# Optimization experiments

Measured on AMD Instinct MI355X. Metric: run time of the kernel, lower is better.

The kernel has to match this reference:

```python
import jax, jax.numpy as jnp
import numpy as np

N, E, D, O, STEP = 100000, 640000, 128, 64, 10


def setup_inputs() -> dict:
    key = jax.random.key(0)
    k1, k2, k3, k4, k5 = jax.random.split(key, 5)
    x = jax.random.normal(k1, (N, D), dtype=jnp.float32)
    edge_index = jax.random.randint(k2, (2, E), 0, N, dtype=jnp.int64)
    t = jax.random.normal(k3, (STEP, D), dtype=jnp.float32)
    W = jax.random.normal(k4, (O, D), dtype=jnp.float32) * 0.05
    b = jax.random.normal(k5, (O,), dtype=jnp.float32) * 0.05
    return {"x": x, "edge_index": edge_index, "t": t, "W": W, "b": b}


def reference(x, edge_index, t, W, b):
    n = x.shape[0]
    # add self loops
    loops = jnp.arange(n, dtype=edge_index.dtype)
    row = jnp.concatenate([edge_index[0], loops])  # source (x_j)
    col = jnp.concatenate([edge_index[1], loops])  # target (aggregation index)
    # symmetric normalization: deg computed over col (targets)
    deg = jax.ops.segment_sum(jnp.ones_like(row, dtype=x.dtype), col, num_segments=n)
    dinv = deg ** -0.5  # deg >= 1 thanks to self loops
    norm = (dinv[row] * dinv[col])[:, None]  # [E+N, 1]
    # per-channel softmax over the 10 hop weights
    t_norm = jax.nn.softmax(t, axis=0)  # [STEP, D]

    def hop(carry, tk):
        h, y = carry
        h = jax.ops.segment_sum(norm * h[row], col, num_segments=n)  # SpMM hop
        return (h, y + tk * h), None

    (_, y), _ = jax.lax.scan(hop, (x, t_norm[0] * x), t_norm[1:])
    return y @ W.T + b
```

## Files before the change

### kernel.cpp

```cpp
#include <hip/hip_runtime.h>

typedef _Float16 half2_t __attribute__((ext_vector_type(2)));
typedef unsigned int uint;

#define D 128
#define O 64
#define UNR 8

static inline size_t align_up(size_t x, size_t a) { return (x + a - 1) & ~(a - 1); }

__device__ __forceinline__ uint pack_f16(float a, float b) {
  half2_t h;
  h.x = (_Float16)a;
  h.y = (_Float16)b;
  return *(uint*)&h;
}

__device__ __forceinline__ float dot2f(uint a, uint b, float c) {
#if defined(__has_builtin) && __has_builtin(__builtin_amdgcn_fdot2)
  return __builtin_amdgcn_fdot2(*(half2_t*)&a, *(half2_t*)&b, c, false);
#else
  half2_t ha = *(half2_t*)&a, hb = *(half2_t*)&b;
  return c + (float)ha.x * (float)hb.x + (float)ha.y * (float)hb.y;
#endif
}


__global__ void count_deg_k(const int* __restrict__ col, int* __restrict__ deg, int E, int n) {
  int i = blockIdx.x * blockDim.x + threadIdx.x;
  if (i >= E) return;
  int c = col[i];
  if ((unsigned)c >= (unsigned)n) return;
  atomicAdd(&deg[c], 1);
}

__global__ void scan1_k(const int* __restrict__ deg, int* __restrict__ row_ptr,
                        int* __restrict__ bsum, float* __restrict__ dinv, int n) {
  __shared__ int s[256];
  int tid = threadIdx.x;
  int gid = blockIdx.x * 256 + tid;
  int dg = (gid < n) ? deg[gid] : 0;
  if (gid < n) dinv[gid] = rsqrtf((float)(dg + 1));
  s[tid] = dg;
  __syncthreads();
  for (int off = 1; off < 256; off <<= 1) {
    int t = (tid >= off) ? s[tid - off] : 0;
    __syncthreads();
    s[tid] += t;
    __syncthreads();
  }
  if (gid < n) row_ptr[gid] = s[tid] - dg;
  if (tid == 255) bsum[blockIdx.x] = s[255];
}

__global__ void scan2_k(int* __restrict__ bsum, int nb) {
  __shared__ int s[512];
  int tid = threadIdx.x;
  int v = (tid < nb) ? bsum[tid] : 0;
  s[tid] = v;
  __syncthreads();
  for (int off = 1; off < 512; off <<= 1) {
    int t = (tid >= off) ? s[tid - off] : 0;
    __syncthreads();
    s[tid] += t;
    __syncthreads();
  }
  if (tid < nb) bsum[tid] = s[tid] - v;
}

__global__ void scan3_k(const int* __restrict__ bsum, const int* __restrict__ deg,
                        int* __restrict__ row_ptr, int* __restrict__ cursor, int n) {
  int gid = blockIdx.x * 256 + threadIdx.x;
  if (gid < n) {
    int r = row_ptr[gid] + bsum[blockIdx.x];
    row_ptr[gid] = r;
    cursor[gid] = r;
    if (gid == n - 1) row_ptr[n] = r + deg[gid];
  }
}

__global__ void fill_k(const int* __restrict__ rows, const int* __restrict__ cols,
                       int* __restrict__ cursor, const float* __restrict__ dinv,
                       int2* __restrict__ csr, int E, int n) {
  int i = blockIdx.x * blockDim.x + threadIdx.x;
  if (i >= E) return;
  int u = rows[i], v = cols[i];
  if ((unsigned)v >= (unsigned)n) return;
  if ((unsigned)u >= (unsigned)n) u = 0;
  int slot = atomicAdd(&cursor[v], 1);
  float nrm = dinv[u] * dinv[v];
  csr[slot] = make_int2(u, __float_as_int(nrm));
}

__global__ void prep_k(const float* __restrict__ t, float* __restrict__ tn,
                       const float* __restrict__ W, uint* __restrict__ Wpk, int step) {
  int tid = threadIdx.x;
  if (tid < D) {
    float vals[16];
    float m = -1e30f;
    for (int k = 0; k < step; ++k) { vals[k] = t[k * D + tid]; m = fmaxf(m, vals[k]); }
    float ssum = 0.f;
    for (int k = 0; k < step; ++k) { vals[k] = expf(vals[k] - m); ssum += vals[k]; }
    float inv = 1.f / ssum;
    for (int k = 0; k < step; ++k) tn[k * D + tid] = vals[k] * inv;
  }
  for (int i = tid; i < O * 64; i += 256) {
    int o = i & 63, dd = i >> 6;
    Wpk[i] = pack_f16(W[o * D + 2 * dd], W[o * D + 2 * dd + 1]);
  }
}

__global__ void init_h_k(const float* __restrict__ x, uint* __restrict__ h0, int total) {
  int i = blockIdx.x * blockDim.x + threadIdx.x;
  if (i >= total) return;
  float2 v = ((const float2*)x)[i];
  h0[i] = pack_f16(v.x, v.y);
}


template <int DO_Y>
__global__ __launch_bounds__(256) void hop_f_k(
    const uint* __restrict__ h_old, uint* __restrict__ h_new, uint* __restrict__ y,
    const int* __restrict__ row_ptr, const int2* __restrict__ csr,
    const float* __restrict__ dinv, const float* __restrict__ tprev,
    const float* __restrict__ tcur, int n) {
  int wid = (blockIdx.x * blockDim.x + threadIdx.x) >> 6;
  int lane = threadIdx.x & 63;
  if (wid >= n) return;
  int v = __builtin_amdgcn_readfirstlane(wid);
  float dv = dinv[v];
  float ns = dv * dv;
  uint hp = h_old[(size_t)v * 64 + lane];
  half2_t hv = *(half2_t*)&hp;
  float hx = (float)hv.x, hy = (float)hv.y;
  float ax = ns * hx, ay = ns * hy;
  int beg = __builtin_amdgcn_readfirstlane(row_ptr[v]);
  int end = __builtin_amdgcn_readfirstlane(row_ptr[v + 1]);
  for (int i = beg; i < end; i += UNR) {
    int u[UNR];
    float w[UNR];
#pragma unroll
    for (int j = 0; j < UNR; ++j) {
      int ic = i + j;
      int icl = (ic < end - 1) ? ic : (end - 1);
      int2 e = csr[icl];
      u[j] = e.x;
      w[j] = (ic < end) ? __int_as_float(e.y) : 0.f;
    }
    uint g[UNR];
#pragma unroll
    for (int j = 0; j < UNR; ++j) g[j] = h_old[(size_t)u[j] * 64 + lane];
#pragma unroll
    for (int j = 0; j < UNR; ++j) {
      half2_t h = *(half2_t*)&g[j];
      ax += w[j] * (float)h.x;
      ay += w[j] * (float)h.y;
    }
  }
  h_new[(size_t)v * 64 + lane] = pack_f16(ax, ay);
  if (DO_Y) {
    float yx = 0.f, yy = 0.f;
    if (DO_Y != 3) {
      float2 ta = ((const float2*)tprev)[lane];
      yx = ta.x * hx;
      yy = ta.y * hy;
    }
    float2 tb = ((const float2*)tcur)[lane];
    yx += tb.x * ax;
    yy += tb.y * ay;
    if (DO_Y >= 2) {
      uint yo = y[(size_t)v * 64 + lane];
      half2_t yh = *(half2_t*)&yo;
      yx += (float)yh.x;
      yy += (float)yh.y;
    }
    y[(size_t)v * 64 + lane] = pack_f16(yx, yy);
  }
}


#define PNW 8

__global__ __launch_bounds__(256) void proj_y2_k(
    const uint* __restrict__ y, const uint* __restrict__ Wpk,
    const float* __restrict__ b, float* __restrict__ out, int n) {
  __shared__ uint sy[4][64];
  int tid = threadIdx.x;
  int lane = tid & 63, wv = tid >> 6;
  uint wreg[64];
#pragma unroll
  for (int j = 0; j < 64; ++j) wreg[j] = Wpk[j * 64 + lane];
  float bias = b[lane];
  int wid = (blockIdx.x * blockDim.x + tid) >> 6;
  int vb = wid * PNW;
  int ve = vb + PNW < n ? vb + PNW : n;
  for (int v = vb; v < ve; ++v) {
    sy[wv][lane] = y[(size_t)v * 64 + lane];
    float acc = bias;
#pragma unroll
    for (int q = 0; q < 16; ++q) {
      uint4 yq = *(const uint4*)&sy[wv][q * 4];
      acc = dot2f(yq.x, wreg[q * 4 + 0], acc);
      acc = dot2f(yq.y, wreg[q * 4 + 1], acc);
      acc = dot2f(yq.z, wreg[q * 4 + 2], acc);
      acc = dot2f(yq.w, wreg[q * 4 + 3], acc);
    }
    out[(size_t)v * O + lane] = acc;
  }
}


extern "C" void kernel_launch(void* const* d_in, const int* in_sizes, int n_in,
                              void* d_out, int out_size, void* d_ws, size_t ws_size,
                              hipStream_t stream) {
  const float* x = (const float*)d_in[0];
  const int* ei = (const int*)d_in[1];
  const float* t = (const float*)d_in[2];
  const float* W = (const float*)d_in[3];
  const float* b = (const float*)d_in[4];
  float* out = (float*)d_out;

  int n = in_sizes[0] / D;
  int E = in_sizes[1] / 2;
  int step = in_sizes[2] / D;
  const int* rows = ei;
  const int* cols = ei + E;

  char* p = (char*)d_ws;
  auto alloc = [&](size_t bytes) { char* r = p; p += align_up(bytes, 256); return r; };
  int*   deg     = (int*)alloc((size_t)n * 4);
  float* dinv    = (float*)alloc((size_t)n * 4);
  int*   row_ptr = (int*)alloc((size_t)(n + 1) * 4);
  int*   cursor  = (int*)alloc((size_t)n * 4);
  int*   bsum    = (int*)alloc(2048);
  int2*  csr     = (int2*)alloc((size_t)E * 8);
  float* tn      = (float*)alloc((size_t)step * D * 4);
  uint*  Wpk     = (uint*)alloc((size_t)O * 64 * 4);

  size_t NS = (size_t)n * 64;
  uint* h_a  = (uint*)alloc(NS * 4);
  uint* h_b  = (uint*)alloc(NS * 4);
  uint* ybuf = (uint*)alloc(NS * 4);

  hipMemsetAsync(deg, 0, (size_t)n * 4, stream);
  int nb1 = (n + 255) / 256;
  count_deg_k<<<(E + 255) / 256, 256, 0, stream>>>(cols, deg, E, n);
  scan1_k<<<nb1, 256, 0, stream>>>(deg, row_ptr, bsum, dinv, n);
  scan2_k<<<1, 512, 0, stream>>>(bsum, nb1);
  scan3_k<<<nb1, 256, 0, stream>>>(bsum, deg, row_ptr, cursor, n);
  fill_k<<<(E + 255) / 256, 256, 0, stream>>>(rows, cols, cursor, dinv, csr, E, n);
  prep_k<<<1, 256, 0, stream>>>(t, tn, W, Wpk, step);

  int hop_blocks = (n + 3) / 4;
  int proj_blocks = (n + PNW * 4 - 1) / (PNW * 4);

  init_h_k<<<((size_t)NS + 255) / 256, 256, 0, stream>>>(x, h_a, (int)NS);
  uint* ho = h_a;
  uint* hn = h_b;
  for (int k = 1; k < step; ++k) {
    const float* tp = tn + (size_t)(k - 1) * D;
    const float* tc = tn + (size_t)k * D;
    if (k & 1) {
      if (k == 1)
        hop_f_k<1><<<hop_blocks, 256, 0, stream>>>(ho, hn, ybuf, row_ptr, csr, dinv, tp, tc, n);
      else
        hop_f_k<2><<<hop_blocks, 256, 0, stream>>>(ho, hn, ybuf, row_ptr, csr, dinv, tp, tc, n);
    } else if (k == step - 1) {
      hop_f_k<3><<<hop_blocks, 256, 0, stream>>>(ho, hn, ybuf, row_ptr, csr, dinv, tp, tc, n);
    } else {
      hop_f_k<0><<<hop_blocks, 256, 0, stream>>>(ho, hn, ybuf, row_ptr, csr, dinv, tp, tc, n);
    }
    uint* tmp = ho; ho = hn; hn = tmp;
  }

  proj_y2_k<<<proj_blocks, 256, 0, stream>>>(ybuf, Wpk, b, out, n);
}
```

Baseline: 526.2 us.

## Process multiple nodes per wavefront with merged edge stream and prefetching

```diff
diff --git a/kernel.cpp b/kernel.cpp
--- a/kernel.cpp
+++ b/kernel.cpp
@@ -6,6 +6,8 @@
 #define D 128
 #define O 64
 #define UNR 8
+#define NPW 8
+#define PNW 8
 
 static inline size_t align_up(size_t x, size_t a) { return (x + a - 1) & ~(a - 1); }
 
@@ -119,67 +121,117 @@
 
 
 template <int DO_Y>
-__global__ __launch_bounds__(256) void hop_f_k(
-    const uint* __restrict__ h_old, uint* __restrict__ h_new, uint* __restrict__ y,
+__global__ __launch_bounds__(256) void hop_m_k(
+    const uint* __restrict__ hsrc, uint* __restrict__ hdst, uint* __restrict__ y,
     const int* __restrict__ row_ptr, const int2* __restrict__ csr,
     const float* __restrict__ dinv, const float* __restrict__ tprev,
     const float* __restrict__ tcur, int n) {
   int wid = (blockIdx.x * blockDim.x + threadIdx.x) >> 6;
   int lane = threadIdx.x & 63;
-  if (wid >= n) return;
-  int v = __builtin_amdgcn_readfirstlane(wid);
-  float dv = dinv[v];
-  float ns = dv * dv;
-  uint hp = h_old[(size_t)v * 64 + lane];
-  half2_t hv = *(half2_t*)&hp;
-  float hx = (float)hv.x, hy = (float)hv.y;
-  float ax = ns * hx, ay = ns * hy;
-  int beg = __builtin_amdgcn_readfirstlane(row_ptr[v]);
-  int end = __builtin_amdgcn_readfirstlane(row_ptr[v + 1]);
-  for (int i = beg; i < end; i += UNR) {
-    int u[UNR];
+  int v0 = wid * NPW;
+  if (v0 >= n) return;
+  int vN = (v0 + NPW < n) ? v0 + NPW : n;
+
+  float2 ta = make_float2(0.f, 0.f), tb = make_float2(0.f, 0.f);
+  if (DO_Y) {
+    if (DO_Y != 3) ta = ((const float2*)tprev)[lane];
+    tb = ((const float2*)tcur)[lane];
+  }
+
+  int vcur = v0;
+  uint hc = hsrc[(v0 << 6) + lane];
+  float dvc = dinv[v0];
+  uint yc = 0, yn = 0;
+  if (DO_Y >= 2) yc = y[(v0 << 6) + lane];
+  int v1c = (v0 + 1 < vN) ? v0 + 1 : vN - 1;
+  uint hn = hsrc[(v1c << 6) + lane];
+  float dvn = dinv[v1c];
+  if (DO_Y >= 2) yn = y[(v1c << 6) + lane];
+
+  int eBeg = __builtin_amdgcn_readfirstlane(row_ptr[v0]);
+  int eEnd = __builtin_amdgcn_readfirstlane(row_ptr[vN]);
+  int nend = __builtin_amdgcn_readfirstlane(row_ptr[v0 + 1]);
+  int v2c = (v0 + 2 <= n) ? v0 + 2 : n;
+  int nefly = row_ptr[v2c];
+
+  float hcx, hcy;
+  { half2_t h = *(half2_t*)&hc; hcx = (float)h.x; hcy = (float)h.y; }
+  float accx = 0.f, accy = 0.f;
+
+#define FLUSH()                                                              \
+  {                                                                          \
+    float ns = dvc * dvc;                                                    \
+    float fx = accx + ns * hcx, fy = accy + ns * hcy;                        \
+    hdst[(vcur << 6) + lane] = pack_f16(fx, fy);                             \
+    if (DO_Y) {                                                              \
+      float yx, yy;                                                          \
+      if (DO_Y == 3) {                                                       \
+        yx = tb.x * fx; yy = tb.y * fy;                                      \
+      } else {                                                               \
+        yx = ta.x * hcx + tb.x * fx;                                         \
+        yy = ta.y * hcy + tb.y * fy;                                         \
+      }                                                                      \
+      if (DO_Y >= 2) {                                                       \
+        half2_t yh = *(half2_t*)&yc;                                         \
+        yx += (float)yh.x; yy += (float)yh.y;                                \
+      }                                                                      \
+      y[(vcur << 6) + lane] = pack_f16(yx, yy);                              \
+    }                                                                        \
+    accx = 0.f; accy = 0.f;                                                  \
+    vcur++;                                                                  \
+    hc = hn; dvc = dvn;                                                      \
+    if (DO_Y >= 2) yc = yn;                                                  \
+    { half2_t h = *(half2_t*)&hc; hcx = (float)h.x; hcy = (float)h.y; }      \
+    int vp = (vcur + 1 < vN) ? vcur + 1 : vN - 1;                            \
+    hn = hsrc[(vp << 6) + lane];                                             \
+    dvn = dinv[vp];                                                          \
+    if (DO_Y >= 2) yn = y[(vp << 6) + lane];                                 \
+    nend = __builtin_amdgcn_readfirstlane(nefly);                            \
+    int v2 = (vcur + 2 <= n) ? vcur + 2 : n;                                 \
+    nefly = row_ptr[v2];                                                     \
+  }
+
+  int2 eb[UNR];
+  if (eBeg < eEnd) {
+#pragma unroll
+    for (int j = 0; j < UNR; ++j) {
+      int ic = eBeg + j;
+      if (ic > eEnd - 1) ic = eEnd - 1;
+      eb[j] = csr[ic];
+    }
+  }
+
+  for (int e = eBeg; e < eEnd; e += UNR) {
+    uint g[UNR];
+#pragma unroll
+    for (int j = 0; j < UNR; ++j) g[j] = hsrc[(eb[j].x << 6) + lane];
     float w[UNR];
 #pragma unroll
+    for (int j = 0; j < UNR; ++j) w[j] = __int_as_float(eb[j].y);
+    int2 nb[UNR];
+#pragma unroll
     for (int j = 0; j < UNR; ++j) {
-      int ic = i + j;
-      int icl = (ic < end - 1) ? ic : (end - 1);
-      int2 e = csr[icl];
-      u[j] = e.x;
-      w[j] = (ic < end) ? __int_as_float(e.y) : 0.f;
-    }
-    uint g[UNR];
-#pragma unroll
-    for (int j = 0; j < UNR; ++j) g[j] = h_old[(size_t)u[j] * 64 + lane];
+      int ic = e + UNR + j;
+      if (ic > eEnd - 1) ic = eEnd - 1;
+      nb[j] = csr[ic];
+    }
 #pragma unroll
     for (int j = 0; j < UNR; ++j) {
-      half2_t h = *(half2_t*)&g[j];
-      ax += w[j] * (float)h.x;
-      ay += w[j] * (float)h.y;
-    }
-  }
-  h_new[(size_t)v * 64 + lane] = pack_f16(ax, ay);
-  if (DO_Y) {
-    float yx = 0.f, yy = 0.f;
-    if (DO_Y != 3) {
-      float2 ta = ((const float2*)tprev)[lane];
-      yx = ta.x * hx;
-      yy = ta.y * hy;
-    }
-    float2 tb = ((const float2*)tcur)[lane];
-    yx += tb.x * ax;
-    yy += tb.y * ay;
-    if (DO_Y >= 2) {
-      uint yo = y[(size_t)v * 64 + lane];
-      half2_t yh = *(half2_t*)&yo;
-      yx += (float)yh.x;
-      yy += (float)yh.y;
-    }
-    y[(size_t)v * 64 + lane] = pack_f16(yx, yy);
-  }
-}
-
-
-#define PNW 8
+      int eid = e + j;
+      if (eid < eEnd) {
+        while (vcur < vN - 1 && nend == eid) { FLUSH(); }
+        half2_t h = *(half2_t*)&g[j];
+        accx += w[j] * (float)h.x;
+        accy += w[j] * (float)h.y;
+      }
+    }
+#pragma unroll
+    for (int j = 0; j < UNR; ++j) eb[j] = nb[j];
+  }
+  while (vcur < vN) { FLUSH(); }
+#undef FLUSH
+}
+
 
 __global__ __launch_bounds__(256) void proj_y2_k(
     const uint* __restrict__ y, const uint* __restrict__ Wpk,
@@ -251,7 +303,7 @@
   fill_k<<<(E + 255) / 256, 256, 0, stream>>>(rows, cols, cursor, dinv, csr, E, n);
   prep_k<<<1, 256, 0, stream>>>(t, tn, W, Wpk, step);
 
-  int hop_blocks = (n + 3) / 4;
+  int hop_blocks = (n + NPW * 4 - 1) / (NPW * 4);
   int proj_blocks = (n + PNW * 4 - 1) / (PNW * 4);
 
   init_h_k<<<((size_t)NS + 255) / 256, 256, 0, stream>>>(x, h_a, (int)NS);
@@ -262,13 +314,13 @@
     const float* tc = tn + (size_t)k * D;
     if (k & 1) {
       if (k == 1)
-        hop_f_k<1><<<hop_blocks, 256, 0, stream>>>(ho, hn, ybuf, row_ptr, csr, dinv, tp, tc, n);
+        hop_m_k<1><<<hop_blocks, 256, 0, stream>>>(ho, hn, ybuf, row_ptr, csr, dinv, tp, tc, n);
       else
-        hop_f_k<2><<<hop_blocks, 256, 0, stream>>>(ho, hn, ybuf, row_ptr, csr, dinv, tp, tc, n);
+        hop_m_k<2><<<hop_blocks, 256, 0, stream>>>(ho, hn, ybuf, row_ptr, csr, dinv, tp, tc, n);
     } else if (k == step - 1) {
-      hop_f_k<3><<<hop_blocks, 256, 0, stream>>>(ho, hn, ybuf, row_ptr, csr, dinv, tp, tc, n);
+      hop_m_k<3><<<hop_blocks, 256, 0, stream>>>(ho, hn, ybuf, row_ptr, csr, dinv, tp, tc, n);
     } else {
-      hop_f_k<0><<<hop_blocks, 256, 0, stream>>>(ho, hn, ybuf, row_ptr, csr, dinv, tp, tc, n);
+      hop_m_k<0><<<hop_blocks, 256, 0, stream>>>(ho, hn, ybuf, row_ptr, csr, dinv, tp, tc, n);
     }
     uint* tmp = ho; ho = hn; hn = tmp;
   }
```

After: 525.7 us. Within noise of the previous version (-0.1%).

## Fuse all propagation hops into a persistent cooperative kernel with LDS-resident y

Applied to the files above, without the earlier changes.

```diff
diff --git a/kernel.cpp b/kernel.cpp
--- a/kernel.cpp
+++ b/kernel.cpp
@@ -1,4 +1,7 @@
 #include <hip/hip_runtime.h>
+#include <hip/hip_cooperative_groups.h>
+
+namespace cg = cooperative_groups;
 
 typedef _Float16 half2_t __attribute__((ext_vector_type(2)));
 typedef unsigned int uint;
@@ -6,6 +9,9 @@
 #define D 128
 #define O 64
 #define UNR 8
+#define NPW 8
+#define PNW 8
+#define NPW_MAX 18
 
 static inline size_t align_up(size_t x, size_t a) { return (x + a - 1) & ~(a - 1); }
 
@@ -118,68 +124,162 @@
 }
 
 
+__global__ __launch_bounds__(256) void coop_hops_k(
+    const float* __restrict__ x,
+    uint* __restrict__ h_a, uint* __restrict__ h_b,
+    const int* __restrict__ row_ptr, const int2* __restrict__ csr,
+    const float* __restrict__ dinv, const float* __restrict__ tn,
+    uint* __restrict__ ybuf, int n, int step, int npw) {
+  cg::grid_group gg = cg::this_grid();
+  __shared__ uint ylds[4 * NPW_MAX * 64];
+  int tid = threadIdx.x;
+  int lane = tid & 63;
+  int wv = tid >> 6;
+  int wid = blockIdx.x * 4 + wv;
+  int v0 = wid * npw;
+  int vN = v0 + npw;
+  if (vN > n) vN = n;
+  int blkBase = blockIdx.x * 4 * npw;
+
+  for (int v = v0; v < vN; ++v) {
+    float2 xv = ((const float2*)x)[((size_t)v << 6) + lane];
+    h_a[((size_t)v << 6) + lane] = pack_f16(xv.x, xv.y);
+    ylds[((v - blkBase) << 6) + lane] = 0;
+  }
+  gg.sync();
+
+  uint* ho = h_a;
+  uint* hn = h_b;
+  for (int k = 1; k < step; ++k) {
+    bool pair = (k & 1) != 0;
+    bool tail = !pair && (k == step - 1);
+    if (v0 < n) {
+      float2 ta = make_float2(0.f, 0.f), tb = make_float2(0.f, 0.f);
+      if (pair) ta = ((const float2*)(tn + (size_t)(k - 1) * D))[lane];
+      if (pair || tail) tb = ((const float2*)(tn + (size_t)k * D))[lane];
+      for (int v = v0; v < vN; ++v) {
+        float dv = dinv[v];
+        float ns = dv * dv;
+        uint hp = ho[((size_t)v << 6) + lane];
+        half2_t hv = *(half2_t*)&hp;
+        float hx = (float)hv.x, hy = (float)hv.y;
+        float ax = ns * hx, ay = ns * hy;
+        int beg = __builtin_amdgcn_readfirstlane(row_ptr[v]);
+        int end = __builtin_amdgcn_readfirstlane(row_ptr[v + 1]);
+        for (int i = beg; i < end; i += UNR) {
+          int u[UNR];
+          float w[UNR];
+#pragma unroll
+          for (int j = 0; j < UNR; ++j) {
+            int ic = i + j;
+            int icl = (ic < end - 1) ? ic : (end - 1);
+            int2 e = csr[icl];
+            u[j] = e.x;
+            w[j] = (ic < end) ? __int_as_float(e.y) : 0.f;
+          }
+          uint g[UNR];
+#pragma unroll
+          for (int j = 0; j < UNR; ++j) g[j] = ho[((size_t)u[j] << 6) + lane];
+#pragma unroll
+          for (int j = 0; j < UNR; ++j) {
+            half2_t h = *(half2_t*)&g[j];
+            ax += w[j] * (float)h.x;
+            ay += w[j] * (float)h.y;
+          }
+        }
+        hn[((size_t)v << 6) + lane] = pack_f16(ax, ay);
+        if (pair || tail) {
+          int slot = ((v - blkBase) << 6) + lane;
+          uint yo = ylds[slot];
+          half2_t yh = *(half2_t*)&yo;
+          float yx = (float)yh.x, yy = (float)yh.y;
+          if (pair) {
+            yx += ta.x * hx + tb.x * ax;
+            yy += ta.y * hy + tb.y * ay;
+          } else {
+            yx += tb.x * ax;
+            yy += tb.y * ay;
+          }
+          ylds[slot] = pack_f16(yx, yy);
+        }
+      }
+    }
+    gg.sync();
+    uint* tmp = ho; ho = hn; hn = tmp;
+  }
+
+  for (int v = v0; v < vN; ++v)
+    ybuf[((size_t)v << 6) + lane] = ylds[((v - blkBase) << 6) + lane];
+}
+
+
 template <int DO_Y>
-__global__ __launch_bounds__(256) void hop_f_k(
-    const uint* __restrict__ h_old, uint* __restrict__ h_new, uint* __restrict__ y,
+__global__ __launch_bounds__(256) void hop_m_k(
+    const uint* __restrict__ hsrc, uint* __restrict__ hdst, uint* __restrict__ y,
     const int* __restrict__ row_ptr, const int2* __restrict__ csr,
     const float* __restrict__ dinv, const float* __restrict__ tprev,
     const float* __restrict__ tcur, int n) {
   int wid = (blockIdx.x * blockDim.x + threadIdx.x) >> 6;
   int lane = threadIdx.x & 63;
-  if (wid >= n) return;
-  int v = __builtin_amdgcn_readfirstlane(wid);
-  float dv = dinv[v];
-  float ns = dv * dv;
-  uint hp = h_old[(size_t)v * 64 + lane];
-  half2_t hv = *(half2_t*)&hp;
-  float hx = (float)hv.x, hy = (float)hv.y;
-  float ax = ns * hx, ay = ns * hy;
-  int beg = __builtin_amdgcn_readfirstlane(row_ptr[v]);
-  int end = __builtin_amdgcn_readfirstlane(row_ptr[v + 1]);
-  for (int i = beg; i < end; i += UNR) {
-    int u[UNR];
-    float w[UNR];
-#pragma unroll
-    for (int j = 0; j < UNR; ++j) {
-      int ic = i + j;
-      int icl = (ic < end - 1) ? ic : (end - 1);
-      int2 e = csr[icl];
-      u[j] = e.x;
-      w[j] = (ic < end) ? __int_as_float(e.y) : 0.f;
-    }
-    uint g[UNR];
-#pragma unroll
-    for (int j = 0; j < UNR; ++j) g[j] = h_old[(size_t)u[j] * 64 + lane];
-#pragma unroll
-    for (int j = 0; j < UNR; ++j) {
-      half2_t h = *(half2_t*)&g[j];
-      ax += w[j] * (float)h.x;
-      ay += w[j] * (float)h.y;
-    }
-  }
-  h_new[(size_t)v * 64 + lane] = pack_f16(ax, ay);
+  int v0 = wid * NPW;
+  if (v0 >= n) return;
+  int vN = (v0 + NPW < n) ? v0 + NPW : n;
+
+  float2 ta = make_float2(0.f, 0.f), tb = make_float2(0.f, 0.f);
   if (DO_Y) {
-    float yx = 0.f, yy = 0.f;
-    if (DO_Y != 3) {
-      float2 ta = ((const float2*)tprev)[lane];
-      yx = ta.x * hx;
-      yy = ta.y * hy;
-    }
-    float2 tb = ((const float2*)tcur)[lane];
-    yx += tb.x * ax;
-    yy += tb.y * ay;
-    if (DO_Y >= 2) {
-      uint yo = y[(size_t)v * 64 + lane];
-      half2_t yh = *(half2_t*)&yo;
-      yx += (float)yh.x;
-      yy += (float)yh.y;
-    }
-    y[(size_t)v * 64 + lane] = pack_f16(yx, yy);
-  }
-}
-
-
-#define PNW 8
+    if (DO_Y != 3) ta = ((const float2*)tprev)[lane];
+    tb = ((const float2*)tcur)[lane];
+  }
+  for (int v = v0; v < vN; ++v) {
+    float dv = dinv[v];
+    float ns = dv * dv;
+    uint hp = hsrc[((size_t)v << 6) + lane];
+    half2_t hv = *(half2_t*)&hp;
+    float hx = (float)hv.x, hy = (float)hv.y;
+    float ax = ns * hx, ay = ns * hy;
+    int beg = __builtin_amdgcn_readfirstlane(row_ptr[v]);
+    int end = __builtin_amdgcn_readfirstlane(row_ptr[v + 1]);
+    for (int i = beg; i < end; i += UNR) {
+      int u[UNR];
+      float w[UNR];
+#pragma unroll
+      for (int j = 0; j < UNR; ++j) {
+        int ic = i + j;
+        int icl = (ic < end - 1) ? ic : (end - 1);
+        int2 e = csr[icl];
+        u[j] = e.x;
+        w[j] = (ic < end) ? __int_as_float(e.y) : 0.f;
+      }
+      uint g[UNR];
+#pragma unroll
+      for (int j = 0; j < UNR; ++j) g[j] = hsrc[((size_t)u[j] << 6) + lane];
+#pragma unroll
+      for (int j = 0; j < UNR; ++j) {
+        half2_t h = *(half2_t*)&g[j];
+        ax += w[j] * (float)h.x;
+        ay += w[j] * (float)h.y;
+      }
+    }
+    hdst[((size_t)v << 6) + lane] = pack_f16(ax, ay);
+    if (DO_Y) {
+      float yx, yy;
+      if (DO_Y == 3) {
+        yx = tb.x * ax; yy = tb.y * ay;
+      } else {
+        yx = ta.x * hx + tb.x * ax;
+        yy = ta.y * hy + tb.y * ay;
+      }
+      if (DO_Y >= 2) {
+        uint yo = y[((size_t)v << 6) + lane];
+        half2_t yh = *(half2_t*)&yo;
+        yx += (float)yh.x;
+        yy += (float)yh.y;
+      }
+      y[((size_t)v << 6) + lane] = pack_f16(yx, yy);
+    }
+  }
+}
+
 
 __global__ __launch_bounds__(256) void proj_y2_k(
     const uint* __restrict__ y, const uint* __restrict__ Wpk,
@@ -251,26 +351,54 @@
   fill_k<<<(E + 255) / 256, 256, 0, stream>>>(rows, cols, cursor, dinv, csr, E, n);
   prep_k<<<1, 256, 0, stream>>>(t, tn, W, Wpk, step);
 
-  int hop_blocks = (n + 3) / 4;
+  static int g_blocks = -2;
+  if (g_blocks == -2) {
+    int coop = 0, dev = 0;
+    hipGetDevice(&dev);
+    if (hipDeviceGetAttribute(&coop, hipDeviceAttributeCooperativeLaunch, dev) != hipSuccess)
+      coop = 0;
+    if (!coop) {
+      g_blocks = -1;
+    } else {
+      int perCU = 0, nCU = 0;
+      hipDeviceGetAttribute(&nCU, hipDeviceAttributeMultiprocessorCount, dev);
+      hipError_t e = hipOccupancyMaxActiveBlocksPerMultiprocessor(
+          &perCU, reinterpret_cast<const void*>(coop_hops_k), 256, 0);
+      g_blocks = (e == hipSuccess && perCU > 0 && nCU > 0) ? perCU * nCU : -1;
+    }
+  }
+
+  int npw = (g_blocks > 0) ? (n + g_blocks * 4 - 1) / (g_blocks * 4) : 0;
+  bool use_coop = (g_blocks > 0) && (npw >= 1) && (npw <= NPW_MAX) && (step >= 2) && (step <= 16);
+
   int proj_blocks = (n + PNW * 4 - 1) / (PNW * 4);
 
-  init_h_k<<<((size_t)NS + 255) / 256, 256, 0, stream>>>(x, h_a, (int)NS);
-  uint* ho = h_a;
-  uint* hn = h_b;
-  for (int k = 1; k < step; ++k) {
-    const float* tp = tn + (size_t)(k - 1) * D;
-    const float* tc = tn + (size_t)k * D;
-    if (k & 1) {
-      if (k == 1)
-        hop_f_k<1><<<hop_blocks, 256, 0, stream>>>(ho, hn, ybuf, row_ptr, csr, dinv, tp, tc, n);
-      else
-        hop_f_k<2><<<hop_blocks, 256, 0, stream>>>(ho, hn, ybuf, row_ptr, csr, dinv, tp, tc, n);
-    } else if (k == step - 1) {
-      hop_f_k<3><<<hop_blocks, 256, 0, stream>>>(ho, hn, ybuf, row_ptr, csr, dinv, tp, tc, n);
-    } else {
-      hop_f_k<0><<<hop_blocks, 256, 0, stream>>>(ho, hn, ybuf, row_ptr, csr, dinv, tp, tc, n);
-    }
-    uint* tmp = ho; ho = hn; hn = tmp;
+  if (use_coop) {
+    void* kargs[] = {(void*)&x,   (void*)&h_a, (void*)&h_b,  (void*)&row_ptr,
+                     (void*)&csr, (void*)&dinv, (void*)&tn,  (void*)&ybuf,
+                     (void*)&n,   (void*)&step, (void*)&npw};
+    hipLaunchCooperativeKernel(reinterpret_cast<void*>(coop_hops_k),
+                               dim3(g_blocks), dim3(256), kargs, 0, stream);
+  } else {
+    int hop_blocks = (n + NPW * 4 - 1) / (NPW * 4);
+    init_h_k<<<((size_t)NS + 255) / 256, 256, 0, stream>>>(x, h_a, (int)NS);
+    uint* ho = h_a;
+    uint* hn = h_b;
+    for (int k = 1; k < step; ++k) {
+      const float* tp = tn + (size_t)(k - 1) * D;
+      const float* tc = tn + (size_t)k * D;
+      if (k & 1) {
+        if (k == 1)
+          hop_m_k<1><<<hop_blocks, 256, 0, stream>>>(ho, hn, ybuf, row_ptr, csr, dinv, tp, tc, n);
+        else
+          hop_m_k<2><<<hop_blocks, 256, 0, stream>>>(ho, hn, ybuf, row_ptr, csr, dinv, tp, tc, n);
+      } else if (k == step - 1) {
+        hop_m_k<3><<<hop_blocks, 256, 0, stream>>>(ho, hn, ybuf, row_ptr, csr, dinv, tp, tc, n);
+      } else {
+        hop_m_k<0><<<hop_blocks, 256, 0, stream>>>(ho, hn, ybuf, row_ptr, csr, dinv, tp, tc, n);
+      }
+      uint* tmp = ho; ho = hn; hn = tmp;
+    }
   }
 
   proj_y2_k<<<proj_blocks, 256, 0, stream>>>(ybuf, Wpk, b, out, n);
```

Result: slower. 538.6 us (+2.3%).

## Merge setup kernels and replace three-pass scan with decoupled look-back scan

Applied to the files above, without the earlier changes.

```diff
diff --git a/kernel.cpp b/kernel.cpp
--- a/kernel.cpp
+++ b/kernel.cpp
@@ -2,10 +2,13 @@
 
 typedef _Float16 half2_t __attribute__((ext_vector_type(2)));
 typedef unsigned int uint;
+typedef unsigned long long ull;
 
 #define D 128
 #define O 64
 #define UNR 8
+#define PNW 8
+#define MAX_SCAN_BLOCKS 2000
 
 static inline size_t align_up(size_t x, size_t a) { return (x + a - 1) & ~(a - 1); }
 
@@ -26,13 +29,89 @@
 }
 
 
-__global__ void count_deg_k(const int* __restrict__ col, int* __restrict__ deg, int E, int n) {
-  int i = blockIdx.x * blockDim.x + threadIdx.x;
-  if (i >= E) return;
-  int c = col[i];
-  if ((unsigned)c >= (unsigned)n) return;
-  atomicAdd(&deg[c], 1);
-}
+__global__ __launch_bounds__(256) void setup_k(
+    const float* __restrict__ x, uint* __restrict__ h0, int totalH,
+    const int* __restrict__ col, int* __restrict__ deg, int E, int n,
+    const float* __restrict__ t, float* __restrict__ tn,
+    const float* __restrict__ W, uint* __restrict__ Wpk, int step,
+    int ib, int eb) {
+  int bid = blockIdx.x;
+  int tid = threadIdx.x;
+  if (bid < ib) {
+    int i = bid * 256 + tid;
+    if (i < totalH) {
+      float2 v = ((const float2*)x)[i];
+      h0[i] = pack_f16(v.x, v.y);
+    }
+  } else if (bid < ib + eb) {
+    int i = (bid - ib) * 256 + tid;
+    if (i < E) {
+      int c = col[i];
+      if ((unsigned)c < (unsigned)n) atomicAdd(&deg[c], 1);
+    }
+  } else {
+    if (tid < D) {
+      float vals[16];
+      float m = -1e30f;
+      for (int k = 0; k < step; ++k) { vals[k] = t[k * D + tid]; m = fmaxf(m, vals[k]); }
+      float ssum = 0.f;
+      for (int k = 0; k < step; ++k) { vals[k] = expf(vals[k] - m); ssum += vals[k]; }
+      float inv = 1.f / ssum;
+      for (int k = 0; k < step; ++k) tn[k * D + tid] = vals[k] * inv;
+    }
+    for (int i = tid; i < O * 64; i += 256) {
+      int o = i & 63, dd = i >> 6;
+      Wpk[i] = pack_f16(W[o * D + 2 * dd], W[o * D + 2 * dd + 1]);
+    }
+  }
+}
+
+
+__global__ __launch_bounds__(256) void scan_all_k(
+    const int* __restrict__ deg, int* __restrict__ row_ptr, int* __restrict__ cursor,
+    float* __restrict__ dinv, ull* __restrict__ desc, int n) {
+  __shared__ int s[256];
+  __shared__ int sOff;
+  int tid = threadIdx.x, bid = blockIdx.x;
+  int gid = bid * 256 + tid;
+  int dg = (gid < n) ? deg[gid] : 0;
+  if (gid < n) dinv[gid] = rsqrtf((float)(dg + 1));
+  s[tid] = dg;
+  __syncthreads();
+  for (int off = 1; off < 256; off <<= 1) {
+    int t = (tid >= off) ? s[tid - off] : 0;
+    __syncthreads();
+    s[tid] += t;
+    __syncthreads();
+  }
+  if (tid == 0) {
+    int agg = s[255];
+    ull mine = ((ull)(bid == 0 ? 2u : 1u) << 32) | (uint)agg;
+    atomicExch(&desc[bid], mine);
+    int off = 0;
+    if (bid > 0) {
+      int j = bid - 1;
+      for (;;) {
+        ull d = atomicAdd(&desc[j], 0ULL);
+        uint f = (uint)(d >> 32);
+        if (f == 0) continue;
+        off += (int)(uint)(d & 0xffffffffULL);
+        if (f == 2) break;
+        --j;
+      }
+      atomicExch(&desc[bid], ((ull)2u << 32) | (uint)(off + agg));
+    }
+    sOff = off;
+  }
+  __syncthreads();
+  if (gid < n) {
+    int r = s[tid] - dg + sOff;
+    row_ptr[gid] = r;
+    cursor[gid] = r;
+    if (gid == n - 1) row_ptr[n] = r + dg;
+  }
+}
+
 
 __global__ void scan1_k(const int* __restrict__ deg, int* __restrict__ row_ptr,
                         int* __restrict__ bsum, float* __restrict__ dinv, int n) {
@@ -56,16 +135,22 @@
 __global__ void scan2_k(int* __restrict__ bsum, int nb) {
   __shared__ int s[512];
   int tid = threadIdx.x;
-  int v = (tid < nb) ? bsum[tid] : 0;
-  s[tid] = v;
-  __syncthreads();
-  for (int off = 1; off < 512; off <<= 1) {
-    int t = (tid >= off) ? s[tid - off] : 0;
-    __syncthreads();
-    s[tid] += t;
-    __syncthreads();
-  }
-  if (tid < nb) bsum[tid] = s[tid] - v;
+  int acc = 0;
+  for (int base = 0; base < nb; base += 512) {
+    int v = (base + tid < nb) ? bsum[base + tid] : 0;
+    s[tid] = v;
+    __syncthreads();
+    for (int off = 1; off < 512; off <<= 1) {
+      int t = (tid >= off) ? s[tid - off] : 0;
+      __syncthreads();
+      s[tid] += t;
+      __syncthreads();
+    }
+    if (base + tid < nb) bsum[base + tid] = s[tid] - v + acc;
+    __syncthreads();
+    acc += s[511];
+    __syncthreads();
+  }
 }
 
 __global__ void scan3_k(const int* __restrict__ bsum, const int* __restrict__ deg,
@@ -78,6 +163,7 @@
     if (gid == n - 1) row_ptr[n] = r + deg[gid];
   }
 }
+
 
 __global__ void fill_k(const int* __restrict__ rows, const int* __restrict__ cols,
                        int* __restrict__ cursor, const float* __restrict__ dinv,
@@ -90,31 +176,6 @@
   int slot = atomicAdd(&cursor[v], 1);
   float nrm = dinv[u] * dinv[v];
   csr[slot] = make_int2(u, __float_as_int(nrm));
-}
-
-__global__ void prep_k(const float* __restrict__ t, float* __restrict__ tn,
-                       const float* __restrict__ W, uint* __restrict__ Wpk, int step) {
-  int tid = threadIdx.x;
-  if (tid < D) {
-    float vals[16];
-    float m = -1e30f;
-    for (int k = 0; k < step; ++k) { vals[k] = t[k * D + tid]; m = fmaxf(m, vals[k]); }
-    float ssum = 0.f;
-    for (int k = 0; k < step; ++k) { vals[k] = expf(vals[k] - m); ssum += vals[k]; }
-    float inv = 1.f / ssum;
-    for (int k = 0; k < step; ++k) tn[k * D + tid] = vals[k] * inv;
-  }
-  for (int i = tid; i < O * 64; i += 256) {
-    int o = i & 63, dd = i >> 6;
-    Wpk[i] = pack_f16(W[o * D + 2 * dd], W[o * D + 2 * dd + 1]);
-  }
-}
-
-__global__ void init_h_k(const float* __restrict__ x, uint* __restrict__ h0, int total) {
-  int i = blockIdx.x * blockDim.x + threadIdx.x;
-  if (i >= total) return;
-  float2 v = ((const float2*)x)[i];
-  h0[i] = pack_f16(v.x, v.y);
 }
 
 
@@ -179,8 +240,6 @@
 }
 
 
-#define PNW 8
-
 __global__ __launch_bounds__(256) void proj_y2_k(
     const uint* __restrict__ y, const uint* __restrict__ Wpk,
     const float* __restrict__ b, float* __restrict__ out, int n) {
@@ -226,13 +285,16 @@
   const int* rows = ei;
   const int* cols = ei + E;
 
+  int nb1 = (n + 255) / 256;
+
   char* p = (char*)d_ws;
   auto alloc = [&](size_t bytes) { char* r = p; p += align_up(bytes, 256); return r; };
   int*   deg     = (int*)alloc((size_t)n * 4);
+  ull*   desc    = (ull*)alloc((size_t)nb1 * 8);
   float* dinv    = (float*)alloc((size_t)n * 4);
   int*   row_ptr = (int*)alloc((size_t)(n + 1) * 4);
   int*   cursor  = (int*)alloc((size_t)n * 4);
-  int*   bsum    = (int*)alloc(2048);
+  int*   bsum    = (int*)alloc(align_up((size_t)nb1 * 4, 256));
   int2*  csr     = (int2*)alloc((size_t)E * 8);
   float* tn      = (float*)alloc((size_t)step * D * 4);
   uint*  Wpk     = (uint*)alloc((size_t)O * 64 * 4);
@@ -242,19 +304,25 @@
   uint* h_b  = (uint*)alloc(NS * 4);
   uint* ybuf = (uint*)alloc(NS * 4);
 
-  hipMemsetAsync(deg, 0, (size_t)n * 4, stream);
-  int nb1 = (n + 255) / 256;
-  count_deg_k<<<(E + 255) / 256, 256, 0, stream>>>(cols, deg, E, n);
-  scan1_k<<<nb1, 256, 0, stream>>>(deg, row_ptr, bsum, dinv, n);
-  scan2_k<<<1, 512, 0, stream>>>(bsum, nb1);
-  scan3_k<<<nb1, 256, 0, stream>>>(bsum, deg, row_ptr, cursor, n);
+  size_t zlen = (size_t)((char*)(desc + nb1) - (char*)deg);
+  hipMemsetAsync(deg, 0, zlen, stream);
+
+  int ib = (int)((NS + 255) / 256);
+  int eb = (E + 255) / 256;
+  setup_k<<<ib + eb + 1, 256, 0, stream>>>(x, h_a, (int)NS, cols, deg, E, n,
+                                           t, tn, W, Wpk, step, ib, eb);
+
+  if (nb1 <= MAX_SCAN_BLOCKS) {
+    scan_all_k<<<nb1, 256, 0, stream>>>(deg, row_ptr, cursor, dinv, desc, n);
+  } else {
+    scan1_k<<<nb1, 256, 0, stream>>>(deg, row_ptr, bsum, dinv, n);
+    scan2_k<<<1, 512, 0, stream>>>(bsum, nb1);
+    scan3_k<<<nb1, 256, 0, stream>>>(bsum, deg, row_ptr, cursor, n);
+  }
+
   fill_k<<<(E + 255) / 256, 256, 0, stream>>>(rows, cols, cursor, dinv, csr, E, n);
-  prep_k<<<1, 256, 0, stream>>>(t, tn, W, Wpk, step);
 
   int hop_blocks = (n + 3) / 4;
-  int proj_blocks = (n + PNW * 4 - 1) / (PNW * 4);
-
-  init_h_k<<<((size_t)NS + 255) / 256, 256, 0, stream>>>(x, h_a, (int)NS);
   uint* ho = h_a;
   uint* hn = h_b;
   for (int k = 1; k < step; ++k) {
@@ -273,5 +341,6 @@
     uint* tmp = ho; ho = hn; hn = tmp;
   }
 
+  int proj_blocks = (n + PNW * 4 - 1) / (PNW * 4);
   proj_y2_k<<<proj_blocks, 256, 0, stream>>>(ybuf, Wpk, b, out, n);
 }
```

Measured after the change: 531.0 us. Within noise of the previous version (+0.9%).
